# Performance work log

Measured on AMD Instinct MI355X. Metric: run time of the kernel, lower is better.

The kernel has to match this reference:

```python
import jax, jax.numpy as jnp
import numpy as np

B, S, D = 2, 2048, 2048
H = 16
HD = D // H
FF = 8192
EPS = 1e-5


def _layer_norm(x, g, b):
    mu = jnp.mean(x, axis=-1, keepdims=True)
    var = jnp.mean(jnp.square(x - mu), axis=-1, keepdims=True)
    return (x - mu) * jax.lax.rsqrt(var + EPS) * g + b


def setup_inputs() -> dict:
    key = jax.random.key(0)
    ks = jax.random.split(key, 8)
    s = 0.02
    return {
        "x": jax.random.normal(ks[0], (B, S, D), dtype=jnp.float32),
        "ln1_g": jnp.ones((D,), jnp.float32),
        "ln1_b": jnp.zeros((D,), jnp.float32),
        "qkv_w": jax.random.normal(ks[1], (D, 3 * D), dtype=jnp.float32) * s,
        "qkv_b": jnp.zeros((3 * D,), jnp.float32),
        "out_w": jax.random.normal(ks[2], (D, D), dtype=jnp.float32) * s,
        "out_b": jnp.zeros((D,), jnp.float32),
        "ln2_g": jnp.ones((D,), jnp.float32),
        "ln2_b": jnp.zeros((D,), jnp.float32),
        "w1": jax.random.normal(ks[3], (D, FF), dtype=jnp.float32) * s,
        "b1": jnp.zeros((FF,), jnp.float32),
        "w2": jax.random.normal(ks[4], (FF, D), dtype=jnp.float32) * s,
        "b2": jnp.zeros((D,), jnp.float32),
    }


def reference(x, ln1_g, ln1_b, qkv_w, qkv_b, out_w, out_b, ln2_g, ln2_b, w1, b1, w2, b2):
    # --- attention sub-block (pre-norm) ---
    residual = x
    h = _layer_norm(x, ln1_g, ln1_b)
    qkv = h @ qkv_w + qkv_b                      # [B,S,3D]
    q, k, v = jnp.split(qkv, 3, axis=-1)
    # [B,S,D] -> [B,H,S,HD]
    q = q.reshape(B, S, H, HD).transpose(0, 2, 1, 3)
    k = k.reshape(B, S, H, HD).transpose(0, 2, 1, 3)
    v = v.reshape(B, S, H, HD).transpose(0, 2, 1, 3)
    scores = jnp.einsum("bhqd,bhkd->bhqk", q, k)  # [B,H,S,S]
    causal = jnp.triu(jnp.ones((S, S), dtype=bool), k=1)
    scores = jnp.where(causal[None, None], -jnp.inf, scores)
    attn = jax.nn.softmax(scores / np.sqrt(HD).astype(np.float32), axis=-1)
    av = jnp.einsum("bhqk,bhkd->bhqd", attn, v)   # [B,H,S,HD]
    av = av.transpose(0, 2, 1, 3).reshape(B, S, D)
    x = residual + (av @ out_w + out_b)
    # --- FFN sub-block (pre-norm) ---
    residual = x
    h = _layer_norm(x, ln2_g, ln2_b)
    h = jax.nn.gelu(h @ w1 + b1, approximate=False)
    x = residual + (h @ w2 + b2)
    return x
```

## Files before the change

kernel.cpp:

```cpp
#include <hip/hip_runtime.h>
#include <hip/hip_bf16.h>

#define B_  2
#define S_  2048
#define D_  2048
#define H_  16
#define HD_ 128
#define FF_ 8192

typedef __bf16 bf16x8 __attribute__((ext_vector_type(8)));
typedef float  f32x4  __attribute__((ext_vector_type(4)));
typedef unsigned short u16;
typedef u16 u16x8 __attribute__((ext_vector_type(8)));

__device__ __forceinline__ u16 f2bf(float f) {
    union { float f; unsigned u; } c; c.f = f;
    unsigned u = c.u;
    u += 0x7fffu + ((u >> 16) & 1u);
    return (u16)(u >> 16);
}

__device__ __forceinline__ void gld16(void* lds, const void* g) {
    __builtin_amdgcn_global_load_lds(
        (const __attribute__((address_space(1))) unsigned int*)g,
        (__attribute__((address_space(3))) unsigned int*)lds,
        16, 0, 0);
}

__global__ __launch_bounds__(256)
void ln_kernel(const float* __restrict__ x, const float* __restrict__ g,
               const float* __restrict__ bb, u16* __restrict__ out)
{
    int row = blockIdx.x, tid = threadIdx.x;
    const float4* xr = (const float4*)(x + (size_t)row * D_);
    float4 a = xr[tid], c = xr[tid + 256];
    float s  = a.x + a.y + a.z + a.w + c.x + c.y + c.z + c.w;
    float s2 = a.x*a.x + a.y*a.y + a.z*a.z + a.w*a.w
             + c.x*c.x + c.y*c.y + c.z*c.z + c.w*c.w;
    #pragma unroll
    for (int off = 32; off > 0; off >>= 1) {
        s  += __shfl_down(s,  off, 64);
        s2 += __shfl_down(s2, off, 64);
    }
    __shared__ float red[16];
    __shared__ float mr[2];
    int wid = tid >> 6, lane = tid & 63;
    if (lane == 0) { red[wid] = s; red[8 + wid] = s2; }
    __syncthreads();
    if (tid == 0) {
        float ts = red[0] + red[1] + red[2] + red[3];
        float t2 = red[8] + red[9] + red[10] + red[11];
        float mu = ts * (1.0f / D_);
        float var = t2 * (1.0f / D_) - mu * mu;
        mr[0] = mu; mr[1] = rsqrtf(var + 1e-5f);
    }
    __syncthreads();
    float mu = mr[0], rstd = mr[1];
    const float4* gg = (const float4*)g;
    const float4* bv = (const float4*)bb;
    float4 g0 = gg[tid], g1 = gg[tid + 256];
    float4 b0 = bv[tid], b1 = bv[tid + 256];
    u16* orow = out + (size_t)row * D_;
    ushort4 o0, o1;
    o0.x = f2bf((a.x - mu) * rstd * g0.x + b0.x);
    o0.y = f2bf((a.y - mu) * rstd * g0.y + b0.y);
    o0.z = f2bf((a.z - mu) * rstd * g0.z + b0.z);
    o0.w = f2bf((a.w - mu) * rstd * g0.w + b0.w);
    o1.x = f2bf((c.x - mu) * rstd * g1.x + b1.x);
    o1.y = f2bf((c.y - mu) * rstd * g1.y + b1.y);
    o1.z = f2bf((c.z - mu) * rstd * g1.z + b1.z);
    o1.w = f2bf((c.w - mu) * rstd * g1.w + b1.w);
    *(ushort4*)&orow[tid * 4]         = o0;
    *(ushort4*)&orow[(tid + 256) * 4] = o1;
}

__global__ __launch_bounds__(256)
void tcvt_kernel(const float* __restrict__ W, u16* __restrict__ WT, int K, int N)
{
    __shared__ float t[32][33];
    int n0 = blockIdx.x << 5, k0 = blockIdx.y << 5;
    int tx = threadIdx.x & 31, ty = threadIdx.x >> 5;
    #pragma unroll
    for (int i = 0; i < 32; i += 8)
        t[ty + i][tx] = W[(size_t)(k0 + ty + i) * N + n0 + tx];
    __syncthreads();
    #pragma unroll
    for (int i = 0; i < 32; i += 8)
        WT[(size_t)(n0 + ty + i) * K + k0 + tx] = f2bf(t[tx][ty + i]);
}

template<int EPI>
__global__ __launch_bounds__(512, 2)
void gemm_kernel(const u16* __restrict__ A, const u16* __restrict__ BT,
                 const float* __restrict__ bias, const float* __restrict__ res,
                 void* __restrict__ outv, int M, int N, int K)
{
    __shared__ u16 ldsA[4 * 4096];
    __shared__ u16 ldsB[4 * 8192];
    (void)M;

    int tid = threadIdx.x;
    int wid = tid >> 6, lane = tid & 63;
    int wm = wid >> 2, wn = wid & 3;
    int quad = lane >> 4, l16 = lane & 15;

    int nwg = (int)gridDim.x;
    int swz = ((int)blockIdx.x & 7) * (nwg >> 3) + ((int)blockIdx.x >> 3);
    int mt = swz & 31;
    int nt = swz >> 5;
    int m0 = mt << 7, n0 = nt << 8;

    int lo3 = (tid & 7) ^ ((tid >> 3) & 7);
    int rS  = ((tid >> 3) << 1) | (lo3 >> 2);
    int cS  = (lo3 & 3) << 3;
    const u16* gA  = A  + (size_t)(m0 + rS) * K + cS;
    const u16* gB0 = BT + (size_t)(n0 + rS) * K + cS;
    const u16* gB1 = gB0 + (size_t)128 * K;

    int slot   = (((l16 & 1) << 2) | quad) ^ (l16 >> 1);
    int laneRd = (l16 >> 1) * 64 + slot * 8;
    int aRd = wm * 2048 + laneRd;
    int bRd = wn * 2048 + laneRd;

    f32x4 acc[4][4] = {};
    bf16x8 af[4];

    auto stA = [&](int b, int ks, int kofs) {
        gld16(ldsA + (b * 2 + ks) * 4096 + wid * 512, gA + kofs);
    };
    auto stB = [&](int b, int ks, int kofs) {
        gld16(ldsB + (b * 2 + ks) * 8192 + wid * 512, gB0 + kofs);
        gld16(ldsB + (b * 2 + ks) * 8192 + 4096 + wid * 512, gB1 + kofs);
    };
    auto phase = [&](int buf, int ks, int nh, bool ar,
                     bool stb, int sb, int sk, int kofs, bool vm) {
        if (ar) {
            #pragma unroll
            for (int t = 0; t < 4; t++)
                af[t] = *(const bf16x8*)(ldsA + (buf * 2 + ks) * 4096 + aRd + t * 512);
        }
        const u16* bp = ldsB + (buf * 2 + ks) * 8192 + bRd + nh * 1024;
        bf16x8 bf0 = *(const bf16x8*)bp;
        bf16x8 bf1 = *(const bf16x8*)(bp + 512);
        if (!stb) stA(sb, sk, kofs); else stB(sb, sk, kofs);
        if (vm) asm volatile("s_waitcnt vmcnt(3)" ::: "memory");
        __builtin_amdgcn_s_barrier();
        asm volatile("s_waitcnt lgkmcnt(0)" ::: "memory");
        __builtin_amdgcn_sched_barrier(0);
        __builtin_amdgcn_s_setprio(1);
        #pragma unroll
        for (int i = 0; i < 4; i++) {
            acc[i][nh * 2 + 0] = __builtin_amdgcn_mfma_f32_16x16x32_bf16(af[i], bf0, acc[i][nh * 2 + 0], 0, 0, 0);
            acc[i][nh * 2 + 1] = __builtin_amdgcn_mfma_f32_16x16x32_bf16(af[i], bf1, acc[i][nh * 2 + 1], 0, 0, 0);
        }
        __builtin_amdgcn_s_setprio(0);
        __builtin_amdgcn_s_barrier();
    };

    int nkt = K >> 6;
    stA(0, 0, 0);  stB(0, 0, 0);
    stA(0, 1, 32); stB(0, 1, 32);
    stA(1, 0, 64); stB(1, 0, 64);
    asm volatile("s_waitcnt vmcnt(3)" ::: "memory");
    __builtin_amdgcn_s_barrier();

    int niter = nkt >> 1;
    for (int it = 0; it < niter; ++it) {
        int t = it << 1;
        int k1 = ((t + 1) << 6) + 32;
        int t2 = t + 2; if (t2 > nkt - 1) t2 = nkt - 1;
        int t3 = t + 3; if (t3 > nkt - 1) t3 = nkt - 1;
        int k2 = t2 << 6, k3 = t3 << 6;
        phase(0, 0, 0, true,  false, 1, 1, k1,      false);
        phase(0, 0, 1, false, true,  1, 1, k1,      false);
        phase(0, 1, 0, true,  false, 0, 0, k2,      false);
        phase(0, 1, 1, false, true,  0, 0, k2,      true);
        phase(1, 0, 0, true,  false, 0, 1, k2 + 32, false);
        phase(1, 0, 1, false, true,  0, 1, k2 + 32, false);
        phase(1, 1, 0, true,  false, 1, 0, k3,      false);
        phase(1, 1, 1, false, true,  1, 0, k3,      true);
    }

    u16*   outb = (u16*)outv;
    float* outf = (float*)outv;
    int colb = n0 + wn * 64, rowb = m0 + wm * 64;
    #pragma unroll
    for (int j = 0; j < 4; j++) {
        int col = colb + j * 16 + l16;
        float bv = bias[col];
        #pragma unroll
        for (int i = 0; i < 4; i++) {
            int row0 = rowb + i * 16 + (quad << 2);
            #pragma unroll
            for (int r = 0; r < 4; r++) {
                float v = acc[i][j][r] + bv;
                size_t idx = (size_t)(row0 + r) * N + col;
                if (EPI == 2) {
                    outf[idx] = v + res[idx];
                } else {
                    if (EPI == 1) v = 0.5f * v * (1.0f + erff(v * 0.70710678118654752f));
                    outb[idx] = f2bf(v);
                }
            }
        }
    }
}

__global__ __launch_bounds__(256, 2)
void attn_kernel(const u16* __restrict__ qkv, u16* __restrict__ av)
{
    __shared__ u16 ldsK[4][64][32];
    __shared__ unsigned ldsVT[128][36];
    __shared__ u16 ldsP[4][32][72];
    int tid = threadIdx.x, wid = tid >> 6, lane = tid & 63;
    int quad = lane >> 4, l16 = lane & 15;
    int bh = blockIdx.y, b = bh >> 4, h = bh & 15;
    int qx = gridDim.x - 1 - blockIdx.x;
    int q0 = qx << 7;
    const u16* base = qkv + (size_t)b * S_ * (3 * D_);

    bf16x8 aq[2][4];
    #pragma unroll
    for (int set = 0; set < 2; set++) {
        int qrow = q0 + set * 64 + wid * 16 + l16;
        const u16* qp = base + (size_t)qrow * (3 * D_) + h * HD_;
        #pragma unroll
        for (int kk = 0; kk < 4; kk++)
            aq[set][kk] = *(const bf16x8*)(qp + kk * 32 + quad * 8);
    }

    float m_i[2][4], l_i[2][4];
    f32x4 oacc[2][8] = {};
    #pragma unroll
    for (int s = 0; s < 2; s++)
        #pragma unroll
        for (int r = 0; r < 4; r++) { m_i[s][r] = -1e30f; l_i[s][r] = 0.f; }

    const float scale = 0.088388347648318447f;
    int ntile = 2 * qx + 2;
    for (int jt = 0; jt < ntile; jt++) {
        int j0 = jt << 6;
        #pragma unroll
        for (int j = 0; j < 4; j++) {
            int c = wid * 4 + j;
            int kk = c >> 2, kb = c & 3;
            int key = (kb << 4) + (lane >> 2);
            const u16* g = base + (size_t)(j0 + key) * (3 * D_) + D_ + h * HD_
                         + kk * 32 + ((lane & 3) << 3);
            gld16((u16*)ldsK + c * 512, g);
        }
        {
            int kp = lane & 31, dhalf = lane >> 5;
            #pragma unroll
            for (int p = 0; p < 2; p++) {
                int doff = wid * 32 + p * 16 + dhalf * 8;
                const u16* g0 = base + (size_t)(j0 + 2 * kp) * (3 * D_)
                              + 2 * D_ + h * HD_ + doff;
                u16x8 v0 = *(const u16x8*)g0;
                u16x8 v1 = *(const u16x8*)(g0 + 3 * D_);
                #pragma unroll
                for (int k = 0; k < 8; k++)
                    ldsVT[doff + k][kp] = (unsigned)v0[k] | ((unsigned)v1[k] << 16);
            }
        }
        __syncthreads();
        f32x4 sacc[2][4] = {};
        #pragma unroll
        for (int kk = 0; kk < 4; kk++)
            #pragma unroll
            for (int n = 0; n < 4; n++) {
                bf16x8 bfr = *(const bf16x8*)&ldsK[kk][(n << 4) + l16][quad << 3];
                sacc[0][n] = __builtin_amdgcn_mfma_f32_16x16x32_bf16(aq[0][kk], bfr, sacc[0][n], 0, 0, 0);
                sacc[1][n] = __builtin_amdgcn_mfma_f32_16x16x32_bf16(aq[1][kk], bfr, sacc[1][n], 0, 0, 0);
            }
        #pragma unroll
        for (int set = 0; set < 2; set++) {
            float rowmax[4] = {-1e30f, -1e30f, -1e30f, -1e30f};
            #pragma unroll
            for (int n = 0; n < 4; n++) {
                int key = j0 + (n << 4) + l16;
                #pragma unroll
                for (int r = 0; r < 4; r++) {
                    float xv = sacc[set][n][r] * scale;
                    int qr = q0 + set * 64 + wid * 16 + (quad << 2) + r;
                    if (key > qr) xv = -1e30f;
                    sacc[set][n][r] = xv;
                    rowmax[r] = fmaxf(rowmax[r], xv);
                }
            }
            #pragma unroll
            for (int off = 1; off < 16; off <<= 1)
                #pragma unroll
                for (int r = 0; r < 4; r++)
                    rowmax[r] = fmaxf(rowmax[r], __shfl_xor(rowmax[r], off, 64));
            float alpha[4], rsum[4];
            #pragma unroll
            for (int r = 0; r < 4; r++) {
                float mn = fmaxf(m_i[set][r], rowmax[r]);
                alpha[r] = __expf(m_i[set][r] - mn);
                m_i[set][r] = mn;
                rsum[r] = 0.f;
            }
            #pragma unroll
            for (int n = 0; n < 4; n++)
                #pragma unroll
                for (int r = 0; r < 4; r++) {
                    float p = __expf(sacc[set][n][r] - m_i[set][r]);
                    rsum[r] += p;
                    ldsP[wid][set * 16 + (quad << 2) + r][(n << 4) + l16] = f2bf(p);
                }
            #pragma unroll
            for (int off = 1; off < 16; off <<= 1)
                #pragma unroll
                for (int r = 0; r < 4; r++)
                    rsum[r] += __shfl_xor(rsum[r], off, 64);
            #pragma unroll
            for (int r = 0; r < 4; r++)
                l_i[set][r] = l_i[set][r] * alpha[r] + rsum[r];
            #pragma unroll
            for (int n = 0; n < 8; n++)
                #pragma unroll
                for (int r = 0; r < 4; r++)
                    oacc[set][n][r] *= alpha[r];
        }
        #pragma unroll
        for (int ks = 0; ks < 2; ks++) {
            bf16x8 pa0 = *(const bf16x8*)&ldsP[wid][l16]     [(ks << 5) + (quad << 3)];
            bf16x8 pa1 = *(const bf16x8*)&ldsP[wid][16 + l16][(ks << 5) + (quad << 3)];
            #pragma unroll
            for (int n = 0; n < 8; n++) {
                bf16x8 vb = *(const bf16x8*)&ldsVT[(n << 4) + l16][(ks << 4) + (quad << 2)];
                oacc[0][n] = __builtin_amdgcn_mfma_f32_16x16x32_bf16(pa0, vb, oacc[0][n], 0, 0, 0);
                oacc[1][n] = __builtin_amdgcn_mfma_f32_16x16x32_bf16(pa1, vb, oacc[1][n], 0, 0, 0);
            }
        }
        __syncthreads();
    }
    #pragma unroll
    for (int set = 0; set < 2; set++)
        #pragma unroll
        for (int r = 0; r < 4; r++) {
            float inv = 1.0f / l_i[set][r];
            int qr = q0 + set * 64 + wid * 16 + (quad << 2) + r;
            u16* op = av + (size_t)(b * S_ + qr) * D_ + h * HD_;
            #pragma unroll
            for (int n = 0; n < 8; n++)
                op[(n << 4) + l16] = f2bf(oacc[set][n][r] * inv);
        }
}

extern "C" void kernel_launch(void* const* d_in, const int* in_sizes, int n_in,
                              void* d_out, int out_size, void* d_ws, size_t ws_size,
                              hipStream_t stream)
{
    const float* x     = (const float*)d_in[0];
    const float* ln1_g = (const float*)d_in[1];
    const float* ln1_b = (const float*)d_in[2];
    const float* qkv_w = (const float*)d_in[3];
    const float* qkv_b = (const float*)d_in[4];
    const float* out_w = (const float*)d_in[5];
    const float* out_b = (const float*)d_in[6];
    const float* ln2_g = (const float*)d_in[7];
    const float* ln2_b = (const float*)d_in[8];
    const float* w1    = (const float*)d_in[9];
    const float* b1    = (const float*)d_in[10];
    const float* w2    = (const float*)d_in[11];
    const float* b2    = (const float*)d_in[12];
    float* out = (float*)d_out;

    char* ws  = (char*)d_ws;
    u16* wT   = (u16*)ws;
    u16* hbuf = (u16*)(ws + (32u << 20));
    u16* big  = (u16*)(ws + (48u << 20));
    u16* qkvb = big;
    u16* ffb  = big;

    dim3 blk(256);
    dim3 gblk(512);

    ln_kernel<<<dim3(B_ * S_), blk, 0, stream>>>(x, ln1_g, ln1_b, hbuf);
    tcvt_kernel<<<dim3(6144 / 32, 2048 / 32), blk, 0, stream>>>(qkv_w, wT, 2048, 6144);
    gemm_kernel<0><<<dim3((6144 / 256) * (4096 / 128)), gblk, 0, stream>>>(
        hbuf, wT, qkv_b, nullptr, (void*)qkvb, 4096, 6144, 2048);
    attn_kernel<<<dim3(S_ / 128, B_ * H_), blk, 0, stream>>>(qkvb, hbuf);
    tcvt_kernel<<<dim3(2048 / 32, 2048 / 32), blk, 0, stream>>>(out_w, wT, 2048, 2048);
    gemm_kernel<2><<<dim3((2048 / 256) * (4096 / 128)), gblk, 0, stream>>>(
        hbuf, wT, out_b, x, (void*)out, 4096, 2048, 2048);
    ln_kernel<<<dim3(B_ * S_), blk, 0, stream>>>(out, ln2_g, ln2_b, hbuf);
    tcvt_kernel<<<dim3(8192 / 32, 2048 / 32), blk, 0, stream>>>(w1, wT, 2048, 8192);
    gemm_kernel<1><<<dim3((8192 / 256) * (4096 / 128)), gblk, 0, stream>>>(
        hbuf, wT, b1, nullptr, (void*)ffb, 4096, 8192, 2048);
    tcvt_kernel<<<dim3(2048 / 32, 8192 / 32), blk, 0, stream>>>(w2, wT, 8192, 2048);
    gemm_kernel<2><<<dim3((2048 / 256) * (4096 / 128)), gblk, 0, stream>>>(
        ffb, wT, b2, out, (void*)out, 4096, 2048, 8192);
}
```

Measured before the change: 1.039 ms.

## Switch GEMM main loop to triple-buffered LDS with full 4x4 MFMA phases

Restructures the bf16 GEMM pipeline from a 2-buffer, 8-phase schedule into a 3-stage ring buffer. Each phase now loads all A and B fragments and issues 16 MFMAs, then prefetches the tile two steps ahead. The vmcnt wait moves after the compute, so global loads have more time to land. This doubles LDS use (about 144KB per block), which may break the launch_bounds(512,2) occupancy target, and it raises register pressure from holding eight fragments at once.

```diff
diff --git a/kernel.cpp b/kernel.cpp
--- a/kernel.cpp
+++ b/kernel.cpp
@@ -95,8 +95,8 @@
                  const float* __restrict__ bias, const float* __restrict__ res,
                  void* __restrict__ outv, int M, int N, int K)
 {
-    __shared__ u16 ldsA[4 * 4096];
-    __shared__ u16 ldsB[4 * 8192];
+    __shared__ u16 ldsA[3 * 8192];
+    __shared__ u16 ldsB[3 * 16384];
     (void)M;
 
     int tid = threadIdx.x;
@@ -123,37 +123,49 @@
     int bRd = wn * 2048 + laneRd;
 
     f32x4 acc[4][4] = {};
-    bf16x8 af[4];
 
     auto stA = [&](int b, int ks, int kofs) {
-        gld16(ldsA + (b * 2 + ks) * 4096 + wid * 512, gA + kofs);
+        gld16(ldsA + b * 8192 + ks * 4096 + wid * 512, gA + kofs);
     };
     auto stB = [&](int b, int ks, int kofs) {
-        gld16(ldsB + (b * 2 + ks) * 8192 + wid * 512, gB0 + kofs);
-        gld16(ldsB + (b * 2 + ks) * 8192 + 4096 + wid * 512, gB1 + kofs);
+        gld16(ldsB + b * 16384 + ks * 8192 + wid * 512, gB0 + kofs);
+        gld16(ldsB + b * 16384 + ks * 8192 + 4096 + wid * 512, gB1 + kofs);
     };
-    auto phase = [&](int buf, int ks, int nh, bool ar,
-                     bool stb, int sb, int sk, int kofs, bool vm) {
-        if (ar) {
-            #pragma unroll
-            for (int t = 0; t < 4; t++)
-                af[t] = *(const bf16x8*)(ldsA + (buf * 2 + ks) * 4096 + aRd + t * 512);
-        }
-        const u16* bp = ldsB + (buf * 2 + ks) * 8192 + bRd + nh * 1024;
-        bf16x8 bf0 = *(const bf16x8*)bp;
+    auto phase = [&](int bt, int ks, int stg, int kofs, bool vm) {
+        const u16* ap = ldsA + bt * 8192 + ks * 4096 + aRd;
+        bf16x8 af0 = *(const bf16x8*)(ap);
+        bf16x8 af1 = *(const bf16x8*)(ap + 512);
+        bf16x8 af2 = *(const bf16x8*)(ap + 1024);
+        bf16x8 af3 = *(const bf16x8*)(ap + 1536);
+        const u16* bp = ldsB + bt * 16384 + ks * 8192 + bRd;
+        bf16x8 bf0 = *(const bf16x8*)(bp);
         bf16x8 bf1 = *(const bf16x8*)(bp + 512);
-        if (!stb) stA(sb, sk, kofs); else stB(sb, sk, kofs);
-        if (vm) asm volatile("s_waitcnt vmcnt(3)" ::: "memory");
+        bf16x8 bf2 = *(const bf16x8*)(bp + 1024);
+        bf16x8 bf3 = *(const bf16x8*)(bp + 1536);
+        stA(stg, ks, kofs);
+        stB(stg, ks, kofs);
         __builtin_amdgcn_s_barrier();
         asm volatile("s_waitcnt lgkmcnt(0)" ::: "memory");
         __builtin_amdgcn_sched_barrier(0);
         __builtin_amdgcn_s_setprio(1);
-        #pragma unroll
-        for (int i = 0; i < 4; i++) {
-            acc[i][nh * 2 + 0] = __builtin_amdgcn_mfma_f32_16x16x32_bf16(af[i], bf0, acc[i][nh * 2 + 0], 0, 0, 0);
-            acc[i][nh * 2 + 1] = __builtin_amdgcn_mfma_f32_16x16x32_bf16(af[i], bf1, acc[i][nh * 2 + 1], 0, 0, 0);
-        }
+        acc[0][0] = __builtin_amdgcn_mfma_f32_16x16x32_bf16(af0, bf0, acc[0][0], 0, 0, 0);
+        acc[0][1] = __builtin_amdgcn_mfma_f32_16x16x32_bf16(af0, bf1, acc[0][1], 0, 0, 0);
+        acc[0][2] = __builtin_amdgcn_mfma_f32_16x16x32_bf16(af0, bf2, acc[0][2], 0, 0, 0);
+        acc[0][3] = __builtin_amdgcn_mfma_f32_16x16x32_bf16(af0, bf3, acc[0][3], 0, 0, 0);
+        acc[1][0] = __builtin_amdgcn_mfma_f32_16x16x32_bf16(af1, bf0, acc[1][0], 0, 0, 0);
+        acc[1][1] = __builtin_amdgcn_mfma_f32_16x16x32_bf16(af1, bf1, acc[1][1], 0, 0, 0);
+        acc[1][2] = __builtin_amdgcn_mfma_f32_16x16x32_bf16(af1, bf2, acc[1][2], 0, 0, 0);
+        acc[1][3] = __builtin_amdgcn_mfma_f32_16x16x32_bf16(af1, bf3, acc[1][3], 0, 0, 0);
+        acc[2][0] = __builtin_amdgcn_mfma_f32_16x16x32_bf16(af2, bf0, acc[2][0], 0, 0, 0);
+        acc[2][1] = __builtin_amdgcn_mfma_f32_16x16x32_bf16(af2, bf1, acc[2][1], 0, 0, 0);
+        acc[2][2] = __builtin_amdgcn_mfma_f32_16x16x32_bf16(af2, bf2, acc[2][2], 0, 0, 0);
+        acc[2][3] = __builtin_amdgcn_mfma_f32_16x16x32_bf16(af2, bf3, acc[2][3], 0, 0, 0);
+        acc[3][0] = __builtin_amdgcn_mfma_f32_16x16x32_bf16(af3, bf0, acc[3][0], 0, 0, 0);
+        acc[3][1] = __builtin_amdgcn_mfma_f32_16x16x32_bf16(af3, bf1, acc[3][1], 0, 0, 0);
+        acc[3][2] = __builtin_amdgcn_mfma_f32_16x16x32_bf16(af3, bf2, acc[3][2], 0, 0, 0);
+        acc[3][3] = __builtin_amdgcn_mfma_f32_16x16x32_bf16(af3, bf3, acc[3][3], 0, 0, 0);
         __builtin_amdgcn_s_setprio(0);
+        if (vm) asm volatile("s_waitcnt vmcnt(6)" ::: "memory");
         __builtin_amdgcn_s_barrier();
     };
 
@@ -161,25 +173,20 @@
     stA(0, 0, 0);  stB(0, 0, 0);
     stA(0, 1, 32); stB(0, 1, 32);
     stA(1, 0, 64); stB(1, 0, 64);
-    asm volatile("s_waitcnt vmcnt(3)" ::: "memory");
+    stA(1, 1, 96); stB(1, 1, 96);
+    asm volatile("s_waitcnt vmcnt(6)" ::: "memory");
     __builtin_amdgcn_s_barrier();
 
-    int niter = nkt >> 1;
-    for (int it = 0; it < niter; ++it) {
-        int t = it << 1;
-        int k1 = ((t + 1) << 6) + 32;
-        int t2 = t + 2; if (t2 > nkt - 1) t2 = nkt - 1;
-        int t3 = t + 3; if (t3 > nkt - 1) t3 = nkt - 1;
-        int k2 = t2 << 6, k3 = t3 << 6;
-        phase(0, 0, 0, true,  false, 1, 1, k1,      false);
-        phase(0, 0, 1, false, true,  1, 1, k1,      false);
-        phase(0, 1, 0, true,  false, 0, 0, k2,      false);
-        phase(0, 1, 1, false, true,  0, 0, k2,      true);
-        phase(1, 0, 0, true,  false, 0, 1, k2 + 32, false);
-        phase(1, 0, 1, false, true,  0, 1, k2 + 32, false);
-        phase(1, 1, 0, true,  false, 1, 0, k3,      false);
-        phase(1, 1, 1, false, true,  1, 0, k3,      true);
-    }
+    int cur = 0;
+    for (int t = 0; t < nkt; ++t) {
+        int stg = cur - 1; if (stg < 0) stg = 2;
+        int tp = t + 2; if (tp > nkt - 1) tp = nkt - 1;
+        int kofs = tp << 6;
+        phase(cur, 0, stg, kofs,      false);
+        phase(cur, 1, stg, kofs + 32, true);
+        cur = cur + 1; if (cur > 2) cur = 0;
+    }
+    asm volatile("s_waitcnt vmcnt(0)" ::: "memory");
 
     u16*   outb = (u16*)outv;
     float* outf = (float*)outv;
```

Measured after the change: 943.5 us. -9.2%, faster.
